# Kernel optimization log

Measured on AMD Instinct MI355X. Metric: run time of the kernel, lower is better.

## Reference

```python
import jax, jax.numpy as jnp
import numpy as np

KH, KW, PAD, G = 3, 3, 1, 4  # kernel, padding, deformable groups


def _bilinear_gather(xg, py, px):
    """xg: [B,G,C,Hin,Win]; py,px: [B,G,K,H,W] sample coords.
    Returns [B,G,C,K,H,W] with zero padding outside the image (mmcv semantics)."""
    B, Gd, C, Hin, Win = xg.shape
    y0 = jnp.floor(py)
    x0 = jnp.floor(px)
    wy1 = py - y0
    wx1 = px - x0
    wy0 = 1.0 - wy1
    wx0 = 1.0 - wx1
    xf = xg.reshape(B, Gd, C, Hin * Win)

    def gather(yi, xi):
        valid = (yi >= 0) & (yi < Hin) & (xi >= 0) & (xi < Win)
        yc = jnp.clip(yi, 0, Hin - 1).astype(jnp.int32)
        xc = jnp.clip(xi, 0, Win - 1).astype(jnp.int32)
        lin = (yc * Win + xc).reshape(B, Gd, 1, -1)  # [B,G,1,K*H*W]
        v = jnp.take_along_axis(xf, lin, axis=3).reshape(B, Gd, C, *yi.shape[2:])
        return v * valid[:, :, None].astype(xg.dtype)

    return (gather(y0, x0) * (wy0 * wx0)[:, :, None]
            + gather(y0, x0 + 1) * (wy0 * wx1)[:, :, None]
            + gather(y0 + 1, x0) * (wy1 * wx0)[:, :, None]
            + gather(y0 + 1, x0 + 1) * (wy1 * wx1)[:, :, None])


def setup_inputs() -> dict:
    key = jax.random.key(0)
    k1, k2, k3, k4 = jax.random.split(key, 4)
    B, Cin, Cout, H, W = 8, 256, 256, 64, 64
    x = jax.random.normal(k1, (B, Cin, H, W), dtype=jnp.float32)
    shape = jax.random.normal(k2, (B, 4, H, W), dtype=jnp.float32)
    # conv_offset: 1x1 conv, 4 -> G*2*KH*KW = 72 channels, no bias
    w_offset = jax.random.normal(k3, (G * 2 * KH * KW, 4), dtype=jnp.float32) * 0.1
    # conv_adaption: deform conv weight, no bias
    w_deform = jax.random.normal(k4, (Cout, Cin, KH, KW), dtype=jnp.float32) * 0.01
    return {"x": x, "shape": shape, "w_offset": w_offset, "w_deform": w_deform}


def reference(x, shape, w_offset, w_deform):
    B, Cin, H, W = x.shape
    Cout = w_deform.shape[0]
    K = KH * KW
    # 1x1 offset-predicting conv on detached shape
    shape = jax.lax.stop_gradient(shape)
    offset = jnp.einsum('oc,bchw->bohw', w_offset, shape)  # [B, G*2*K, H, W]
    off = offset.reshape(B, G, K, 2, H, W)  # mmcv layout: (dy, dx) per tap
    dy, dx = off[:, :, :, 0], off[:, :, :, 1]  # [B,G,K,H,W]
    # base sampling grid for each kernel tap
    ky, kx = jnp.meshgrid(jnp.arange(KH), jnp.arange(KW), indexing='ij')
    ky = ky.reshape(-1)
    kx = kx.reshape(-1)
    base_y = (ky - PAD)[:, None, None] + jnp.arange(H)[None, :, None]  # [K,H,1]
    base_x = (kx - PAD)[:, None, None] + jnp.arange(W)[None, None, :]  # [K,1,W]
    py = base_y[None, None].astype(x.dtype) + dy  # [B,G,K,H,W]
    px = base_x[None, None].astype(x.dtype) + dx
    xg = x.reshape(B, G, Cin // G, H, W)
    sampled = _bilinear_gather(xg, py, px)  # [B,G,Cpg,K,H,W]
    wr = w_deform.reshape(Cout, G, Cin // G, K)
    out = jnp.einsum('ogck,bgckhw->bohw', wr, sampled)
    return jax.nn.relu(out)
```

## Files before the change

kernel.cpp:

```cpp
#include <hip/hip_runtime.h>
#include <hip/hip_bf16.h>


#define Bn   8
#define CIN  256
#define COUT 256
#define Hn   64
#define Wn   64
#define Gn   4
#define Kn   9
#define CPG  64
#define GK   36

typedef __bf16 bf16x8 __attribute__((ext_vector_type(8)));
typedef float  f32x4  __attribute__((ext_vector_type(4)));

__global__ void fa_xprep(const float* __restrict__ x, __bf16* __restrict__ xt) {
    const int b = blockIdx.x >> 6, tile = blockIdx.x & 63;
    const int hw0 = tile * 64;
    const int t = threadIdx.x;
    __shared__ __bf16 sm[64][264];
    const int hw4 = t & 15, cq = t >> 4;
#pragma unroll
    for (int it = 0; it < 16; it++) {
        int c = it * 16 + cq;
        float4 v = *(const float4*)&x[((size_t)(b * CIN + c)) * 4096 + hw0 + hw4 * 4];
        sm[hw4 * 4 + 0][c] = (__bf16)v.x;
        sm[hw4 * 4 + 1][c] = (__bf16)v.y;
        sm[hw4 * 4 + 2][c] = (__bf16)v.z;
        sm[hw4 * 4 + 3][c] = (__bf16)v.w;
    }
    __syncthreads();
#pragma unroll
    for (int j = 0; j < 8; j++) {
        int hw = j * 8 + (t >> 5), seg = t & 31;
        bf16x8 v;
#pragma unroll
        for (int u = 0; u < 8; u++) v[u] = sm[hw][seg * 8 + u];
        *(bf16x8*)&xt[((size_t)b * 4096 + hw0 + hw) * 256 + seg * 8] = v;
    }
}

__global__ void fa_wprep(const float* __restrict__ w, __bf16* __restrict__ wfrag) {
    int i = blockIdx.x * 256 + threadIdx.x;
    if (i >= GK * 16 * 2 * 512) return;
    int j    = i & 7;
    int lane = (i >> 3) & 63;
    int ks   = (i >> 9) & 1;
    int mt   = (i >> 10) & 15;
    int gk   = i >> 14;
    int g = gk / Kn, k = gk - g * Kn;
    int o = mt * 16 + (lane & 15);
    int c = ks * 32 + (lane >> 4) * 8 + j;
    wfrag[i] = (__bf16)w[(size_t)(o * CIN + g * CPG + c) * Kn + k];
}

__global__ __launch_bounds__(256, 4)
void fa_main(const __bf16* __restrict__ xt, const float* __restrict__ shp,
             const float* __restrict__ w_off, const __bf16* __restrict__ wfrag,
             float* __restrict__ out) {
    const int blk = blockIdx.x;
    const int b = blk >> 7, h = (blk >> 1) & 63, wh = blk & 1;
    const int w0 = wh * 32;
    const int t = threadIdx.x;
    const int wid = t >> 6, lane = t & 63;
    const int col = lane & 15, quad = lane >> 4;
    const int cg = t & 7, wl = t >> 3;

    __shared__ int   s_iyx[GK * 32];
    __shared__ float s_fy[GK * 32];
    __shared__ float s_fx[GK * 32];
    __shared__ __align__(16) __bf16 sB[2][32 * 64];

    for (int i = t; i < GK * 32; i += 256) {
        int gk = i >> 5, w = (i & 31) + w0;
        int g = gk / Kn, k = gk - g * Kn;
        int ky = k / 3, kx = k - ky * 3;
        int oy = (g * Kn + k) * 2;
        float dy = 0.f, dx = 0.f;
#pragma unroll
        for (int c = 0; c < 4; c++) {
            float sv = shp[((b * 4 + c) * Hn + h) * Wn + w];
            dy = fmaf(w_off[(oy    ) * 4 + c], sv, dy);
            dx = fmaf(w_off[(oy + 1) * 4 + c], sv, dx);
        }
        float py = (float)(h + ky - 1) + dy;
        float px = (float)(w + kx - 1) + dx;
        float y0 = floorf(py), x0 = floorf(px);
        s_fy[i] = py - y0;
        s_fx[i] = px - x0;
        s_iyx[i] = (((int)y0 & 0xffff) << 16) | ((int)x0 & 0xffff);
    }

    const __bf16* xb = xt + (size_t)b * 4096 * 256;

    auto issue = [&](int gk, bf16x8* c4, float* w4) {
        int m = gk * 32 + wl;
        int g = gk / Kn;
        int pk = s_iyx[m];
        int iy = pk >> 16, ix = (pk << 16) >> 16;
        float fy = s_fy[m], fx = s_fx[m];
        bool y0v = (unsigned)iy       < (unsigned)Hn;
        bool y1v = (unsigned)(iy + 1) < (unsigned)Hn;
        bool x0v = (unsigned)ix       < (unsigned)Wn;
        bool x1v = (unsigned)(ix + 1) < (unsigned)Wn;
        int yc0 = min(max(iy, 0), Hn - 1), yc1 = min(max(iy + 1, 0), Hn - 1);
        int xc0 = min(max(ix, 0), Wn - 1), xc1 = min(max(ix + 1, 0), Wn - 1);
        const __bf16* base = xb + g * CPG + cg * 8;
        c4[0] = *(const bf16x8*)(base + ((size_t)(yc0 * 64 + xc0)) * 256);
        c4[1] = *(const bf16x8*)(base + ((size_t)(yc0 * 64 + xc1)) * 256);
        c4[2] = *(const bf16x8*)(base + ((size_t)(yc1 * 64 + xc0)) * 256);
        c4[3] = *(const bf16x8*)(base + ((size_t)(yc1 * 64 + xc1)) * 256);
        float wy1 = fy, wy0 = 1.f - fy, wx1 = fx, wx0 = 1.f - fx;
        w4[0] = (y0v && x0v) ? wy0 * wx0 : 0.f;
        w4[1] = (y0v && x1v) ? wy0 * wx1 : 0.f;
        w4[2] = (y1v && x0v) ? wy1 * wx0 : 0.f;
        w4[3] = (y1v && x1v) ? wy1 * wx1 : 0.f;
    };
    auto commit = [&](const bf16x8* c4, const float* w4, int buf) {
        bf16x8 r;
#pragma unroll
        for (int j = 0; j < 8; j++) {
            float v = w4[0] * (float)c4[0][j] + w4[1] * (float)c4[1][j]
                    + w4[2] * (float)c4[2][j] + w4[3] * (float)c4[3][j];
            r[j] = (__bf16)v;
        }
        *(bf16x8*)&sB[buf][(wl * 8 + (cg ^ (wl & 7))) * 8] = r;
    };

    f32x4 acc[4][2];
#pragma unroll
    for (int mt = 0; mt < 4; mt++)
#pragma unroll
        for (int nt = 0; nt < 2; nt++) acc[mt][nt] = (f32x4){0.f, 0.f, 0.f, 0.f};

    __syncthreads();

    {
        bf16x8 c4[4]; float w4[4];
        issue(0, c4, w4);
        commit(c4, w4, 0);
    }
    __syncthreads();

    bf16x8 c4[4]; float w4[4];
    for (int gk = 0; gk < GK; gk++) {
        const int buf = gk & 1;
        const __bf16* wbase = wfrag + (((size_t)gk * 16 + wid * 4) * 2) * 512;
        bf16x8 af[2][4];
#pragma unroll
        for (int ks = 0; ks < 2; ks++)
#pragma unroll
            for (int mt = 0; mt < 4; mt++)
                af[ks][mt] = *(const bf16x8*)(wbase + ((size_t)(mt * 2 + ks) * 64 + lane) * 8);
        if (gk + 1 < GK) issue(gk + 1, c4, w4);
#pragma unroll
        for (int ks = 0; ks < 2; ks++) {
            bf16x8 bfv[2];
#pragma unroll
            for (int nt = 0; nt < 2; nt++) {
                int w = nt * 16 + col;
                int cq8 = ks * 4 + quad;
                bfv[nt] = *(const bf16x8*)&sB[buf][(w * 8 + (cq8 ^ (w & 7))) * 8];
            }
#pragma unroll
            for (int mt = 0; mt < 4; mt++)
#pragma unroll
                for (int nt = 0; nt < 2; nt++)
                    acc[mt][nt] = __builtin_amdgcn_mfma_f32_16x16x32_bf16(
                        af[ks][mt], bfv[nt], acc[mt][nt], 0, 0, 0);
        }
        if (gk + 1 < GK) commit(c4, w4, buf ^ 1);
        __syncthreads();
    }

#pragma unroll
    for (int mt = 0; mt < 4; mt++)
#pragma unroll
        for (int r = 0; r < 4; r++) {
            int o = wid * 64 + mt * 16 + quad * 4 + r;
            float* rowp = out + (((size_t)b * COUT + o) * Hn + h) * Wn + w0;
#pragma unroll
            for (int nt = 0; nt < 2; nt++)
                rowp[nt * 16 + col] = fmaxf(acc[mt][nt][r], 0.f);
        }
}

extern "C" void kernel_launch(void* const* d_in, const int* in_sizes, int n_in,
                              void* d_out, int out_size, void* d_ws, size_t ws_size,
                              hipStream_t stream) {
    const float* x     = (const float*)d_in[0];
    const float* shp   = (const float*)d_in[1];
    const float* w_off = (const float*)d_in[2];
    const float* w_def = (const float*)d_in[3];
    float* out = (float*)d_out;
    __bf16* wfrag = (__bf16*)d_ws;
    __bf16* xt    = (__bf16*)((char*)d_ws + (2u << 20));

    fa_xprep<<<Bn * 64, 256, 0, stream>>>(x, xt);
    int nT = GK * 16 * 2 * 512;
    fa_wprep<<<(nT + 255) / 256, 256, 0, stream>>>(w_def, wfrag);
    fa_main<<<Bn * Hn * 2, 256, 0, stream>>>(xt, shp, w_off, wfrag, out);
}
```

Measured before the change: 160.9 us.

## Widen main tile to two batches, deepen gather pipeline, merge prep kernels

The main kernel now covers two batch images per block (N tile of 64 columns instead of 32), so each weight fragment loaded from global memory feeds twice as many MFMAs, and the grid shrinks to 512 blocks. The gather pipeline is deepened so loads for step gk+2 are in flight while step gk+1 is committed. The x-transpose and weight-fragment prep kernels are merged into one launch, and the x transpose no longer goes through shared memory. The costs are more registers and LDS per block (launch bounds drop to 2 blocks per SM), fewer blocks available to hide latency, and strided scalar reads in the new x prep path.

Result: faster. 154.7 us (-3.9%).

```diff
diff --git a/kernel.cpp b/kernel.cpp
--- a/kernel.cpp
+++ b/kernel.cpp
@@ -15,65 +15,53 @@
 typedef __bf16 bf16x8 __attribute__((ext_vector_type(8)));
 typedef float  f32x4  __attribute__((ext_vector_type(4)));
 
-__global__ void fa_xprep(const float* __restrict__ x, __bf16* __restrict__ xt) {
-    const int b = blockIdx.x >> 6, tile = blockIdx.x & 63;
-    const int hw0 = tile * 64;
-    const int t = threadIdx.x;
-    __shared__ __bf16 sm[64][264];
-    const int hw4 = t & 15, cq = t >> 4;
-#pragma unroll
-    for (int it = 0; it < 16; it++) {
-        int c = it * 16 + cq;
-        float4 v = *(const float4*)&x[((size_t)(b * CIN + c)) * 4096 + hw0 + hw4 * 4];
-        sm[hw4 * 4 + 0][c] = (__bf16)v.x;
-        sm[hw4 * 4 + 1][c] = (__bf16)v.y;
-        sm[hw4 * 4 + 2][c] = (__bf16)v.z;
-        sm[hw4 * 4 + 3][c] = (__bf16)v.w;
-    }
-    __syncthreads();
-#pragma unroll
-    for (int j = 0; j < 8; j++) {
-        int hw = j * 8 + (t >> 5), seg = t & 31;
+__global__ void fa_prep(const float* __restrict__ x, const float* __restrict__ w,
+                        __bf16* __restrict__ xt, __bf16* __restrict__ wfrag) {
+    const int bid = blockIdx.x, t = threadIdx.x;
+    if (bid < 4096) {
+        const int c8q = bid & 7, hwt = (bid >> 3) & 63, b = bid >> 9;
+        const int hw = hwt * 64 + (t & 63);
+        const int c8 = c8q * 4 + (t >> 6);
+        const float* xp = x + ((size_t)(b * CIN + c8 * 8) << 12) + hw;
         bf16x8 v;
 #pragma unroll
-        for (int u = 0; u < 8; u++) v[u] = sm[hw][seg * 8 + u];
-        *(bf16x8*)&xt[((size_t)b * 4096 + hw0 + hw) * 256 + seg * 8] = v;
+        for (int j = 0; j < 8; j++) v[j] = (__bf16)xp[(size_t)j << 12];
+        *(bf16x8*)&xt[(((size_t)b << 12) + hw) * 256 + c8 * 8] = v;
+    } else {
+        int i = (bid - 4096) * 256 + t;
+        int j    = i & 7;
+        int lane = (i >> 3) & 63;
+        int ks   = (i >> 9) & 1;
+        int mt   = (i >> 10) & 15;
+        int gk   = i >> 14;
+        int g = gk / Kn, k = gk - g * Kn;
+        int o = mt * 16 + (lane & 15);
+        int c = ks * 32 + (lane >> 4) * 8 + j;
+        wfrag[i] = (__bf16)w[(size_t)(o * CIN + g * CPG + c) * Kn + k];
     }
 }
 
-__global__ void fa_wprep(const float* __restrict__ w, __bf16* __restrict__ wfrag) {
-    int i = blockIdx.x * 256 + threadIdx.x;
-    if (i >= GK * 16 * 2 * 512) return;
-    int j    = i & 7;
-    int lane = (i >> 3) & 63;
-    int ks   = (i >> 9) & 1;
-    int mt   = (i >> 10) & 15;
-    int gk   = i >> 14;
-    int g = gk / Kn, k = gk - g * Kn;
-    int o = mt * 16 + (lane & 15);
-    int c = ks * 32 + (lane >> 4) * 8 + j;
-    wfrag[i] = (__bf16)w[(size_t)(o * CIN + g * CPG + c) * Kn + k];
-}
-
-__global__ __launch_bounds__(256, 4)
+__global__ __launch_bounds__(256, 2)
 void fa_main(const __bf16* __restrict__ xt, const float* __restrict__ shp,
              const float* __restrict__ w_off, const __bf16* __restrict__ wfrag,
              float* __restrict__ out) {
     const int blk = blockIdx.x;
-    const int b = blk >> 7, h = (blk >> 1) & 63, wh = blk & 1;
+    const int bp = blk >> 7, h = (blk >> 1) & 63, wh = blk & 1;
     const int w0 = wh * 32;
     const int t = threadIdx.x;
     const int wid = t >> 6, lane = t & 63;
     const int col = lane & 15, quad = lane >> 4;
-    const int cg = t & 7, wl = t >> 3;
-
-    __shared__ int   s_iyx[GK * 32];
-    __shared__ float s_fy[GK * 32];
-    __shared__ float s_fx[GK * 32];
-    __shared__ __align__(16) __bf16 sB[2][32 * 64];
-
-    for (int i = t; i < GK * 32; i += 256) {
-        int gk = i >> 5, w = (i & 31) + w0;
+    const int cg = t & 7, nl0 = t >> 3;
+
+    __shared__ int   s_iyx[GK * 64];
+    __shared__ float s_fy[GK * 64];
+    __shared__ float s_fx[GK * 64];
+    __shared__ __align__(16) __bf16 sB[2][64 * 64];
+
+    for (int i = t; i < GK * 64; i += 256) {
+        int gk = i >> 6, n = i & 63;
+        int bb = n >> 5, w = w0 + (n & 31);
+        int b = bp * 2 + bb;
         int g = gk / Kn, k = gk - g * Kn;
         int ky = k / 3, kx = k - ky * 3;
         int oy = (g * Kn + k) * 2;
@@ -92,58 +80,66 @@
         s_iyx[i] = (((int)y0 & 0xffff) << 16) | ((int)x0 & 0xffff);
     }
 
-    const __bf16* xb = xt + (size_t)b * 4096 * 256;
-
-    auto issue = [&](int gk, bf16x8* c4, float* w4) {
-        int m = gk * 32 + wl;
-        int g = gk / Kn;
-        int pk = s_iyx[m];
-        int iy = pk >> 16, ix = (pk << 16) >> 16;
-        float fy = s_fy[m], fx = s_fx[m];
-        bool y0v = (unsigned)iy       < (unsigned)Hn;
-        bool y1v = (unsigned)(iy + 1) < (unsigned)Hn;
-        bool x0v = (unsigned)ix       < (unsigned)Wn;
-        bool x1v = (unsigned)(ix + 1) < (unsigned)Wn;
-        int yc0 = min(max(iy, 0), Hn - 1), yc1 = min(max(iy + 1, 0), Hn - 1);
-        int xc0 = min(max(ix, 0), Wn - 1), xc1 = min(max(ix + 1, 0), Wn - 1);
-        const __bf16* base = xb + g * CPG + cg * 8;
-        c4[0] = *(const bf16x8*)(base + ((size_t)(yc0 * 64 + xc0)) * 256);
-        c4[1] = *(const bf16x8*)(base + ((size_t)(yc0 * 64 + xc1)) * 256);
-        c4[2] = *(const bf16x8*)(base + ((size_t)(yc1 * 64 + xc0)) * 256);
-        c4[3] = *(const bf16x8*)(base + ((size_t)(yc1 * 64 + xc1)) * 256);
-        float wy1 = fy, wy0 = 1.f - fy, wx1 = fx, wx0 = 1.f - fx;
-        w4[0] = (y0v && x0v) ? wy0 * wx0 : 0.f;
-        w4[1] = (y0v && x1v) ? wy0 * wx1 : 0.f;
-        w4[2] = (y1v && x0v) ? wy1 * wx0 : 0.f;
-        w4[3] = (y1v && x1v) ? wy1 * wx1 : 0.f;
+    bf16x8 c4[2][4];
+    float  w4[2][4];
+
+    auto issue = [&](int gk) {
+#pragma unroll
+        for (int s = 0; s < 2; s++) {
+            int n = nl0 + s * 32;
+            int bb = n >> 5;
+            int b = bp * 2 + bb;
+            int m = gk * 64 + n;
+            int g = gk / Kn;
+            int pk = s_iyx[m];
+            int iy = pk >> 16, ix = (pk << 16) >> 16;
+            float fy = s_fy[m], fx = s_fx[m];
+            bool y0v = (unsigned)iy       < (unsigned)Hn;
+            bool y1v = (unsigned)(iy + 1) < (unsigned)Hn;
+            bool x0v = (unsigned)ix       < (unsigned)Wn;
+            bool x1v = (unsigned)(ix + 1) < (unsigned)Wn;
+            int yc0 = min(max(iy, 0), Hn - 1), yc1 = min(max(iy + 1, 0), Hn - 1);
+            int xc0 = min(max(ix, 0), Wn - 1), xc1 = min(max(ix + 1, 0), Wn - 1);
+            const __bf16* base = xt + (((size_t)b << 12)) * 256 + g * CPG + cg * 8;
+            c4[s][0] = *(const bf16x8*)(base + ((size_t)(yc0 * 64 + xc0)) * 256);
+            c4[s][1] = *(const bf16x8*)(base + ((size_t)(yc0 * 64 + xc1)) * 256);
+            c4[s][2] = *(const bf16x8*)(base + ((size_t)(yc1 * 64 + xc0)) * 256);
+            c4[s][3] = *(const bf16x8*)(base + ((size_t)(yc1 * 64 + xc1)) * 256);
+            float wy1 = fy, wy0 = 1.f - fy, wx1 = fx, wx0 = 1.f - fx;
+            w4[s][0] = (y0v && x0v) ? wy0 * wx0 : 0.f;
+            w4[s][1] = (y0v && x1v) ? wy0 * wx1 : 0.f;
+            w4[s][2] = (y1v && x0v) ? wy1 * wx0 : 0.f;
+            w4[s][3] = (y1v && x1v) ? wy1 * wx1 : 0.f;
+        }
     };
-    auto commit = [&](const bf16x8* c4, const float* w4, int buf) {
-        bf16x8 r;
-#pragma unroll
-        for (int j = 0; j < 8; j++) {
-            float v = w4[0] * (float)c4[0][j] + w4[1] * (float)c4[1][j]
-                    + w4[2] * (float)c4[2][j] + w4[3] * (float)c4[3][j];
-            r[j] = (__bf16)v;
-        }
-        *(bf16x8*)&sB[buf][(wl * 8 + (cg ^ (wl & 7))) * 8] = r;
+    auto commit = [&](int buf) {
+#pragma unroll
+        for (int s = 0; s < 2; s++) {
+            int n = nl0 + s * 32;
+            bf16x8 r;
+#pragma unroll
+            for (int j = 0; j < 8; j++) {
+                float v = w4[s][0] * (float)c4[s][0][j] + w4[s][1] * (float)c4[s][1][j]
+                        + w4[s][2] * (float)c4[s][2][j] + w4[s][3] * (float)c4[s][3][j];
+                r[j] = (__bf16)v;
+            }
+            *(bf16x8*)&sB[buf][(n * 8 + (cg ^ (n & 7))) * 8] = r;
+        }
     };
 
-    f32x4 acc[4][2];
+    f32x4 acc[4][4];
 #pragma unroll
     for (int mt = 0; mt < 4; mt++)
 #pragma unroll
-        for (int nt = 0; nt < 2; nt++) acc[mt][nt] = (f32x4){0.f, 0.f, 0.f, 0.f};
+        for (int nt = 0; nt < 4; nt++) acc[mt][nt] = (f32x4){0.f, 0.f, 0.f, 0.f};
 
     __syncthreads();
 
-    {
-        bf16x8 c4[4]; float w4[4];
-        issue(0, c4, w4);
-        commit(c4, w4, 0);
-    }
+    issue(0);
+    commit(0);
+    issue(1);
     __syncthreads();
 
-    bf16x8 c4[4]; float w4[4];
     for (int gk = 0; gk < GK; gk++) {
         const int buf = gk & 1;
         const __bf16* wbase = wfrag + (((size_t)gk * 16 + wid * 4) * 2) * 512;
@@ -153,24 +149,24 @@
 #pragma unroll
             for (int mt = 0; mt < 4; mt++)
                 af[ks][mt] = *(const bf16x8*)(wbase + ((size_t)(mt * 2 + ks) * 64 + lane) * 8);
-        if (gk + 1 < GK) issue(gk + 1, c4, w4);
+        if (gk + 1 < GK) commit(buf ^ 1);
+        if (gk + 2 < GK) issue(gk + 2);
 #pragma unroll
         for (int ks = 0; ks < 2; ks++) {
-            bf16x8 bfv[2];
-#pragma unroll
-            for (int nt = 0; nt < 2; nt++) {
-                int w = nt * 16 + col;
+            bf16x8 bfv[4];
+#pragma unroll
+            for (int nt = 0; nt < 4; nt++) {
+                int n = nt * 16 + col;
                 int cq8 = ks * 4 + quad;
-                bfv[nt] = *(const bf16x8*)&sB[buf][(w * 8 + (cq8 ^ (w & 7))) * 8];
+                bfv[nt] = *(const bf16x8*)&sB[buf][(n * 8 + (cq8 ^ (n & 7))) * 8];
             }
 #pragma unroll
             for (int mt = 0; mt < 4; mt++)
 #pragma unroll
-                for (int nt = 0; nt < 2; nt++)
+                for (int nt = 0; nt < 4; nt++)
                     acc[mt][nt] = __builtin_amdgcn_mfma_f32_16x16x32_bf16(
                         af[ks][mt], bfv[nt], acc[mt][nt], 0, 0, 0);
         }
-        if (gk + 1 < GK) commit(c4, w4, buf ^ 1);
         __syncthreads();
     }
 
@@ -179,10 +175,14 @@
 #pragma unroll
         for (int r = 0; r < 4; r++) {
             int o = wid * 64 + mt * 16 + quad * 4 + r;
-            float* rowp = out + (((size_t)b * COUT + o) * Hn + h) * Wn + w0;
-#pragma unroll
-            for (int nt = 0; nt < 2; nt++)
-                rowp[nt * 16 + col] = fmaxf(acc[mt][nt][r], 0.f);
+#pragma unroll
+            for (int nt = 0; nt < 4; nt++) {
+                int n = nt * 16 + col;
+                int b = bp * 2 + (n >> 5);
+                int w = w0 + (n & 31);
+                out[(((size_t)(b * COUT + o)) << 12) + h * Wn + w] =
+                    fmaxf(acc[mt][nt][r], 0.f);
+            }
         }
 }
 
@@ -197,8 +197,6 @@
     __bf16* wfrag = (__bf16*)d_ws;
     __bf16* xt    = (__bf16*)((char*)d_ws + (2u << 20));
 
-    fa_xprep<<<Bn * 64, 256, 0, stream>>>(x, xt);
-    int nT = GK * 16 * 2 * 512;
-    fa_wprep<<<(nT + 255) / 256, 256, 0, stream>>>(w_def, wfrag);
-    fa_main<<<Bn * Hn * 2, 256, 0, stream>>>(xt, shp, w_off, wfrag, out);
+    fa_prep<<<4096 + 2304, 256, 0, stream>>>(x, w_def, xt, wfrag);
+    fa_main<<<512, 256, 0, stream>>>(xt, shp, w_off, wfrag, out);
 }
```
